# Optimization experiments

Hardware: AMD Instinct MI355X
Metric: run time of the kernel (lower is better)

Reference implementation:

```python
import jax, jax.numpy as jnp
import numpy as np

N_NODES = 50000
N_EDGES = 800000
IN_CH = 128
HID_CH = 8
OUT_CH = 64
HEADS = 32
NEG_SLOPE = 0.2  # PyG GATConv default


def setup_inputs() -> dict:
    key = jax.random.key(0)
    ks = jax.random.split(key, 12)
    x = jax.random.normal(ks[0], (N_NODES, IN_CH), dtype=jnp.float32)
    # edge_index with no self loops (src != dst), matching PyG's remove_self_loops
    src = jax.random.randint(ks[1], (N_EDGES,), 0, N_NODES)
    off = jax.random.randint(ks[2], (N_EDGES,), 1, N_NODES)
    dst = (src + off) % N_NODES
    edge_index = jnp.stack([src, dst]).astype(jnp.int64)
    s = 0.1
    W1 = jax.random.normal(ks[3], (IN_CH, HEADS * HID_CH), dtype=jnp.float32) * s
    att_src1 = jax.random.normal(ks[4], (HEADS, HID_CH), dtype=jnp.float32) * s
    att_dst1 = jax.random.normal(ks[5], (HEADS, HID_CH), dtype=jnp.float32) * s
    b1 = jnp.zeros((HEADS * HID_CH,), dtype=jnp.float32)
    W2 = jax.random.normal(ks[6], (HEADS * HID_CH, OUT_CH), dtype=jnp.float32) * s
    att_src2 = jax.random.normal(ks[7], (1, OUT_CH), dtype=jnp.float32) * s
    att_dst2 = jax.random.normal(ks[8], (1, OUT_CH), dtype=jnp.float32) * s
    b2 = jnp.zeros((OUT_CH,), dtype=jnp.float32)
    return {"x": x, "edge_index": edge_index, "W1": W1, "att_src1": att_src1,
            "att_dst1": att_dst1, "b1": b1, "W2": W2, "att_src2": att_src2,
            "att_dst2": att_dst2, "b2": b2}


def _gat_conv(x, src, dst, W, a_src, a_dst, bias, concat):
    # Faithful PyG GATConv: linear -> per-edge LeakyReLU score -> segment softmax over dst -> scatter-add
    n = x.shape[0]
    H, C = a_src.shape
    h = (x @ W).reshape(n, H, C)                      # [N,H,C]
    alpha_src = jnp.sum(h * a_src, axis=-1)           # [N,H]
    alpha_dst = jnp.sum(h * a_dst, axis=-1)           # [N,H]
    e = jax.nn.leaky_relu(alpha_src[src] + alpha_dst[dst], negative_slope=NEG_SLOPE)  # [E,H]
    e_max = jax.ops.segment_max(e, dst, num_segments=n)          # every node has a self loop
    ex = jnp.exp(e - e_max[dst])
    denom = jax.ops.segment_sum(ex, dst, num_segments=n)
    alpha = ex / (denom[dst] + 1e-16)                 # [E,H]
    msg = h[src] * alpha[:, :, None]                  # [E,H,C]
    out = jax.ops.segment_sum(msg, dst, num_segments=n)          # [N,H,C]
    out = out.reshape(n, H * C) if concat else out.mean(axis=1)
    return out + bias


def reference(x, edge_index, W1, att_src1, att_dst1, b1, W2, att_src2, att_dst2, b2):
    n = x.shape[0]
    loops = jnp.arange(n, dtype=edge_index.dtype)
    src = jnp.concatenate([edge_index[0], loops])     # add_self_loops (PyG default)
    dst = jnp.concatenate([edge_index[1], loops])
    h = _gat_conv(x, src, dst, W1, att_src1, att_dst1, b1, concat=True)
    h = _gat_conv(h, src, dst, W2, att_src2, att_dst2, b2, concat=False)
    return jax.nn.sigmoid(h)
```

## Files before the change

kernel.cpp:

```cpp
#include <hip/hip_runtime.h>
#include <hip/hip_bf16.h>

constexpr int N  = 50000;
constexpr int E  = 800000;
constexpr int F0 = 128;
constexpr int H1 = 32;
constexpr int F1 = 256;
constexpr int F2 = 64;
constexpr int NB = (N + 255) / 256;
constexpr int NPAD = 782 * 64;
constexpr int W1SZ = F0 * F1;
constexpr int W2SZ = F1 * F2;
constexpr float NEG_SLOPE = 0.2f;

typedef unsigned short u16;
typedef unsigned int   u32;
typedef __attribute__((ext_vector_type(8))) short bf16x8;
typedef __attribute__((ext_vector_type(4))) float f32x4;

__device__ __forceinline__ float leaky(float e) {
    return fmaxf(e, 0.f) + NEG_SLOPE * fminf(e, 0.f);
}
__device__ __forceinline__ float bf2f(u16 u) {
    u32 v = ((u32)u) << 16;
    return __builtin_bit_cast(float, v);
}
__device__ __forceinline__ u16 f2bf(float f) {
    u32 u = __builtin_bit_cast(u32, f);
    u += 0x7fffu + ((u >> 16) & 1u);
    return (u16)(u >> 16);
}
__device__ __forceinline__ u32 pack2(float a, float b) {
    return (u32)f2bf(a) | ((u32)f2bf(b) << 16);
}
__device__ __forceinline__ void up2(u32 v, float& lo, float& hi) {
    lo = __builtin_bit_cast(float, v << 16);
    hi = __builtin_bit_cast(float, v & 0xffff0000u);
}

__global__ void k_detect(const unsigned long long* __restrict__ p, int* __restrict__ flag) {
    __shared__ int bad;
    if (threadIdx.x == 0) bad = 0;
    __syncthreads();
    unsigned long long v = p[threadIdx.x];
    if (v >= (unsigned long long)N) atomicOr(&bad, 1);
    __syncthreads();
    if (threadIdx.x == 0) *flag = bad ? 0 : 1;
}
__device__ __forceinline__ int load_idx(const void* ei, long long i, int is64) {
    return is64 ? (int)((const long long*)ei)[i] : ((const int*)ei)[i];
}

__global__ void k_count(const void* __restrict__ ei, const int* __restrict__ flag,
                        int* __restrict__ deg) {
    int e = blockIdx.x * blockDim.x + threadIdx.x;
    if (e >= E) return;
    int dst = load_idx(ei, (long long)E + e, *flag);
    atomicAdd(&deg[dst], 1);
}
__global__ __launch_bounds__(256) void k_bsum(const int* __restrict__ deg, int* __restrict__ bsum) {
    int b = blockIdx.x, t = threadIdx.x, i = b * 256 + t;
    int v = (i < N) ? deg[i] : 0;
#pragma unroll
    for (int o = 1; o < 64; o <<= 1) v += __shfl_xor(v, o, 64);
    __shared__ int sw[4];
    if ((t & 63) == 0) sw[t >> 6] = v;
    __syncthreads();
    if (t == 0) bsum[b] = sw[0] + sw[1] + sw[2] + sw[3];
}
__global__ __launch_bounds__(256) void k_bscan(int* __restrict__ bsum, int* __restrict__ rsN) {
    int t = threadIdx.x, lane = t & 63, wy = t >> 6;
    int v = (t < NB) ? bsum[t] : 0;
    int inc = v;
#pragma unroll
    for (int o = 1; o < 64; o <<= 1) { int u = __shfl_up(inc, o, 64); if (lane >= o) inc += u; }
    __shared__ int wtot[4];
    if (lane == 63) wtot[wy] = inc;
    __syncthreads();
    int offs = 0;
    for (int k = 0; k < wy; k++) offs += wtot[k];
    int excl = offs + inc - v;
    if (t < NB) bsum[t] = excl;
    if (t == NB - 1) *rsN = excl + v;
}
__global__ __launch_bounds__(256) void k_rs(const int* __restrict__ deg,
                                            const int* __restrict__ bsum, int* __restrict__ rs) {
    int b = blockIdx.x, t = threadIdx.x, i = b * 256 + t;
    int lane = t & 63, wy = t >> 6;
    int v = (i < N) ? deg[i] : 0;
    int inc = v;
#pragma unroll
    for (int o = 1; o < 64; o <<= 1) { int u = __shfl_up(inc, o, 64); if (lane >= o) inc += u; }
    __shared__ int wtot[4];
    if (lane == 63) wtot[wy] = inc;
    __syncthreads();
    int offs = bsum[b];
    for (int k = 0; k < wy; k++) offs += wtot[k];
    if (i < N) rs[i] = offs + inc - v;
}
__global__ void k_scatter(const void* __restrict__ ei, const int* __restrict__ flag,
                          const int* __restrict__ rs, int* __restrict__ fill,
                          int* __restrict__ csr) {
    int e = blockIdx.x * blockDim.x + threadIdx.x;
    if (e >= E) return;
    int is64 = *flag;
    int src = load_idx(ei, e, is64);
    int dst = load_idx(ei, (long long)E + e, is64);
    int pos = rs[dst] + atomicAdd(&fill[dst], 1);
    csr[pos] = src;
}

__global__ __launch_bounds__(256) void k_prepw(
        const float* __restrict__ W1, const float* __restrict__ W2,
        u16* __restrict__ w1t, u16* __restrict__ w2t) {
    int i = blockIdx.x * 256 + threadIdx.x;
    if (i < W1SZ) {
        int n = i >> 7, k = i & 127;
        w1t[(n << 7) + (k ^ ((n & 7) << 3))] = f2bf(W1[k * F1 + n]);
    } else if (i < W1SZ + W2SZ) {
        int j = i - W1SZ;
        int n = j >> 8, k = j & 255;
        w2t[(n << 8) + (k ^ ((n & 7) << 3))] = f2bf(W2[k * F2 + n]);
    }
}

__global__ __launch_bounds__(256) void k_gemm1(
        const float* __restrict__ x, const u16* __restrict__ w1t, u16* __restrict__ h1b) {
    __shared__ u16 As[64 * 128];
    int r0 = blockIdx.x * 64;
    int t = threadIdx.x, w = t >> 6, l = t & 63;
    {
        int r = t >> 2, k0 = (t & 3) * 32, rr = r0 + r;
        int swz = (r & 7) << 3;
        float4 f[8];
        if (rr < N) {
            const float4* px = (const float4*)(x + (size_t)rr * F0 + k0);
#pragma unroll
            for (int j = 0; j < 8; j++) f[j] = px[j];
        } else {
#pragma unroll
            for (int j = 0; j < 8; j++) f[j] = make_float4(0.f, 0.f, 0.f, 0.f);
        }
#pragma unroll
        for (int g = 0; g < 4; g++) {
            uint4 st;
            st.x = pack2(f[2 * g].x, f[2 * g].y);
            st.y = pack2(f[2 * g].z, f[2 * g].w);
            st.z = pack2(f[2 * g + 1].x, f[2 * g + 1].y);
            st.w = pack2(f[2 * g + 1].z, f[2 * g + 1].w);
            *(uint4*)(As + r * 128 + ((k0 + 8 * g) ^ swz)) = st;
        }
    }
    bf16x8 bfrag[4][4];
#pragma unroll
    for (int n = 0; n < 4; n++) {
        int col = w * 64 + n * 16 + (l & 15);
        const u16* wrow = w1t + col * 128;
        int swz = (col & 7) << 3;
#pragma unroll
        for (int ks = 0; ks < 4; ks++)
            bfrag[n][ks] = *(const bf16x8*)(wrow + ((ks * 32 + (l >> 4) * 8) ^ swz));
    }
    __syncthreads();
    f32x4 z = {0.f, 0.f, 0.f, 0.f};
    f32x4 acc[4][4];
#pragma unroll
    for (int m = 0; m < 4; m++)
#pragma unroll
        for (int n = 0; n < 4; n++) acc[m][n] = z;
#pragma unroll
    for (int ks = 0; ks < 4; ks++) {
#pragma unroll
        for (int m = 0; m < 4; m++) {
            int row = m * 16 + (l & 15);
            bf16x8 a = *(const bf16x8*)(As + row * 128 +
                                        ((ks * 32 + (l >> 4) * 8) ^ ((row & 7) << 3)));
#pragma unroll
            for (int n = 0; n < 4; n++)
                acc[m][n] = __builtin_amdgcn_mfma_f32_16x16x32_bf16(a, bfrag[n][ks], acc[m][n], 0, 0, 0);
        }
    }
#pragma unroll
    for (int m = 0; m < 4; m++) {
        int rbase = r0 + m * 16 + (l >> 4) * 4;
#pragma unroll
        for (int n = 0; n < 4; n++) {
            int col = w * 64 + n * 16 + (l & 15);
#pragma unroll
            for (int r = 0; r < 4; r++) {
                int rr = rbase + r;
                if (rr < N) h1b[(size_t)rr * 256 + (col ^ ((rr & 7) << 3))] = f2bf(acc[m][n][r]);
            }
        }
    }
}

__global__ __launch_bounds__(256) void k_alpha1(
        const u16* __restrict__ h1b, const float* __restrict__ as1, const float* __restrict__ ad1,
        float* __restrict__ asrc1, float* __restrict__ adst1) {
    int row = blockIdx.x * 4 + (threadIdx.x >> 6);
    if (row >= N) return;
    int l = threadIdx.x & 63;
    int swz = (row & 7) << 3;
    uint2 v = *(const uint2*)(h1b + (size_t)row * 256 + 4 * l);
    int c0 = (4 * l) ^ swz;
    float f0, f1, f2, f3;
    up2(v.x, f0, f1); up2(v.y, f2, f3);
    float ps = f0 * as1[c0] + f1 * as1[c0 + 1] + f2 * as1[c0 + 2] + f3 * as1[c0 + 3];
    float pd = f0 * ad1[c0] + f1 * ad1[c0 + 1] + f2 * ad1[c0 + 2] + f3 * ad1[c0 + 3];
    ps += __shfl_xor(ps, 1, 64);
    pd += __shfl_xor(pd, 1, 64);
    if (!(l & 1)) {
        int head = (l >> 1) ^ (swz >> 3);
        asrc1[(size_t)row * H1 + head] = ps;
        adst1[(size_t)row * H1 + head] = pd;
    }
}

__global__ __launch_bounds__(256) void k_edge1(
        const int* __restrict__ rs, const int* __restrict__ csr,
        const u16* __restrict__ h1b, const float* __restrict__ asrc,
        const float* __restrict__ adst, const float* __restrict__ b1,
        u16* __restrict__ outb) {
    int d = blockIdx.x * 4 + (threadIdx.x >> 6);
    if (d >= N) return;
    int l = threadIdx.x & 63;
    int hl = l >> 1;
    int beg = rs[d], end = rs[d + 1];
    float ad_sc = adst[(size_t)d * H1 + (l & 31)];
    float wself = __expf(leaky(asrc[(size_t)d * H1 + hl] + adst[(size_t)d * H1 + hl]));
    float den = wself;
    int swzD = (d & 7) << 3;
    uint2 vd = *(const uint2*)(h1b + (size_t)d * 256 + ((4 * l) ^ swzD));
    float a0, a1, a2, a3;
    up2(vd.x, a0, a1); up2(vd.y, a2, a3);
    float c0 = wself * a0, c1 = wself * a1, c2 = wself * a2, c3 = wself * a3;

    for (int base = beg; base < end; base += 64) {
        int cnt = min(64, end - base);
        int s_ch = (base + l < end) ? csr[base + l] : 0;
        for (int i = 0; i < cnt; i += 2) {
            int sA = __shfl(s_ch, i, 64);
            int sB = __shfl(s_ch, i + 1, 64);
            int sS = (l < 32) ? sA : sB;
            float e = leaky(asrc[(size_t)sS * H1 + (l & 31)] + ad_sc);
            bool valid = (l < 32) | (i + 1 < cnt);
            float wsc = valid ? __expf(e) : 0.f;
            float wA = __shfl(wsc, hl, 64);
            float wB = __shfl(wsc, 32 + hl, 64);
            den += wA + wB;
            uint2 va = *(const uint2*)(h1b + (size_t)sA * 256 + ((4 * l) ^ ((sA & 7) << 3)));
            uint2 vb = *(const uint2*)(h1b + (size_t)sB * 256 + ((4 * l) ^ ((sB & 7) << 3)));
            float t0, t1, t2, t3;
            up2(va.x, t0, t1); up2(va.y, t2, t3);
            c0 = fmaf(wA, t0, c0); c1 = fmaf(wA, t1, c1);
            c2 = fmaf(wA, t2, c2); c3 = fmaf(wA, t3, c3);
            up2(vb.x, t0, t1); up2(vb.y, t2, t3);
            c0 = fmaf(wB, t0, c0); c1 = fmaf(wB, t1, c1);
            c2 = fmaf(wB, t2, c2); c3 = fmaf(wB, t3, c3);
        }
    }
    float inv = 1.f / (den + 1e-16f);
    int ch = 4 * l;
    uint2 st;
    st.x = pack2(c0 * inv + b1[ch], c1 * inv + b1[ch + 1]);
    st.y = pack2(c2 * inv + b1[ch + 2], c3 * inv + b1[ch + 3]);
    *(uint2*)(outb + (size_t)d * 256 + (ch ^ swzD)) = st;
}

__global__ __launch_bounds__(256) void k_gemm2(
        const u16* __restrict__ ab, const u16* __restrict__ w2t, u16* __restrict__ h2b) {
    __shared__ u16 As[64 * 256];
    int r0 = blockIdx.x * 64;
    int t = threadIdx.x, w = t >> 6, l = t & 63;
    {
        const uint4* gsrc = (const uint4*)(ab + (size_t)r0 * 256);
        uint4* lds = (uint4*)As;
        for (int i = t; i < 2048; i += 256) lds[i] = gsrc[i];
    }
    __syncthreads();
    f32x4 z = {0.f, 0.f, 0.f, 0.f};
    f32x4 acc[4];
#pragma unroll
    for (int n = 0; n < 4; n++) acc[n] = z;
    int row = w * 16 + (l & 15);
    int swzA = (row & 7) << 3;
#pragma unroll
    for (int ks = 0; ks < 8; ks++) {
        int ka = ks * 32 + (l >> 4) * 8;
        bf16x8 a = *(const bf16x8*)(As + row * 256 + (ka ^ swzA));
#pragma unroll
        for (int n = 0; n < 4; n++) {
            int col = n * 16 + (l & 15);
            bf16x8 b = *(const bf16x8*)(w2t + col * 256 + (ka ^ ((col & 7) << 3)));
            acc[n] = __builtin_amdgcn_mfma_f32_16x16x32_bf16(a, b, acc[n], 0, 0, 0);
        }
    }
#pragma unroll
    for (int n = 0; n < 4; n++) {
        int col = n * 16 + (l & 15);
#pragma unroll
        for (int r = 0; r < 4; r++) {
            int rr = r0 + w * 16 + (l >> 4) * 4 + r;
            if (rr < N) h2b[(size_t)rr * F2 + col] = f2bf(acc[n][r]);
        }
    }
}

__global__ __launch_bounds__(256) void k_alpha2(
        const u16* __restrict__ h2b, const float* __restrict__ a2s, const float* __restrict__ a2d,
        float* __restrict__ asrc2, float* __restrict__ adst2) {
    int row = blockIdx.x * 4 + (threadIdx.x >> 6);
    if (row >= N) return;
    int l = threadIdx.x & 63;
    float f = bf2f(h2b[(size_t)row * F2 + l]);
    float ps = f * a2s[l], pd = f * a2d[l];
#pragma unroll
    for (int o = 1; o < 64; o <<= 1) {
        ps += __shfl_xor(ps, o, 64);
        pd += __shfl_xor(pd, o, 64);
    }
    if (l == 0) { asrc2[row] = ps; adst2[row] = pd; }
}

__global__ __launch_bounds__(256) void k_edge2(
        const int* __restrict__ rs, const int* __restrict__ csr,
        const u16* __restrict__ h2b, const float* __restrict__ asrc,
        const float* __restrict__ adst, const float* __restrict__ b2,
        float* __restrict__ out) {
    int d = blockIdx.x * 4 + (threadIdx.x >> 6);
    if (d >= N) return;
    int l = threadIdx.x & 63;
    int q = l >> 4, c4 = (l & 15) * 4;
    int beg = rs[d], end = rs[d + 1];
    float add_ = adst[d];
    float wself = __expf(leaky(asrc[d] + add_));
    float wq0 = (q == 0) ? wself : 0.f;
    float den = wq0;
    uint2 vd = *(const uint2*)(h2b + (size_t)d * F2 + c4);
    float a0, a1, a2, a3;
    up2(vd.x, a0, a1); up2(vd.y, a2, a3);
    float c0 = wq0 * a0, c1 = wq0 * a1, c2 = wq0 * a2, c3 = wq0 * a3;

    for (int base = beg; base < end; base += 64) {
        int cnt = min(64, end - base);
        bool in = (base + l < end);
        int s_ch = in ? csr[base + l] : 0;
        float w_l = in ? __expf(leaky(asrc[s_ch] + add_)) : 0.f;
        for (int i = 0; i < cnt; i += 4) {
            int e = i + q;
            float wi = __shfl(w_l, e, 64);
            int   si = __shfl(s_ch, e, 64);
            wi = (e < cnt) ? wi : 0.f;
            uint2 v = *(const uint2*)(h2b + (size_t)si * F2 + c4);
            float t0, t1, t2, t3;
            up2(v.x, t0, t1); up2(v.y, t2, t3);
            c0 = fmaf(wi, t0, c0); c1 = fmaf(wi, t1, c1);
            c2 = fmaf(wi, t2, c2); c3 = fmaf(wi, t3, c3);
            den += wi;
        }
    }
    den += __shfl_xor(den, 16, 64); den += __shfl_xor(den, 32, 64);
    c0 += __shfl_xor(c0, 16, 64);   c0 += __shfl_xor(c0, 32, 64);
    c1 += __shfl_xor(c1, 16, 64);   c1 += __shfl_xor(c1, 32, 64);
    c2 += __shfl_xor(c2, 16, 64);   c2 += __shfl_xor(c2, 32, 64);
    c3 += __shfl_xor(c3, 16, 64);   c3 += __shfl_xor(c3, 32, 64);
    if (q == 0) {
        float inv = 1.f / (den + 1e-16f);
        float4 o;
        o.x = 1.f / (1.f + __expf(-(c0 * inv + b2[c4])));
        o.y = 1.f / (1.f + __expf(-(c1 * inv + b2[c4 + 1])));
        o.z = 1.f / (1.f + __expf(-(c2 * inv + b2[c4 + 2])));
        o.w = 1.f / (1.f + __expf(-(c3 * inv + b2[c4 + 3])));
        *(float4*)(out + (size_t)d * F2 + c4) = o;
    }
}

extern "C" void kernel_launch(void* const* d_in, const int* in_sizes, int n_in,
                              void* d_out, int out_size, void* d_ws, size_t ws_size,
                              hipStream_t stream) {
    const float* x   = (const float*)d_in[0];
    const void*  ei  = d_in[1];
    const float* W1  = (const float*)d_in[2];
    const float* as1 = (const float*)d_in[3];
    const float* ad1 = (const float*)d_in[4];
    const float* b1  = (const float*)d_in[5];
    const float* W2  = (const float*)d_in[6];
    const float* a2s = (const float*)d_in[7];
    const float* a2d = (const float*)d_in[8];
    const float* b2  = (const float*)d_in[9];
    float* out = (float*)d_out;

    char* wp = (char*)d_ws;
    size_t off = 0;
    auto alloc = [&](size_t bytes) {
        void* p = wp + off;
        off = (off + bytes + 255) & ~(size_t)255;
        return p;
    };
    int* flag  = (int*)alloc(4);
    int* deg   = (int*)alloc((size_t)N * 4);
    int* fill  = (int*)alloc((size_t)N * 4);
    int* rs    = (int*)alloc((size_t)(N + 1) * 4);
    int* bsum  = (int*)alloc((size_t)NB * 4);
    int* csr   = (int*)alloc((size_t)E * 4);
    u16* w1t   = (u16*)alloc((size_t)W1SZ * 2);
    u16* w2t   = (u16*)alloc((size_t)W2SZ * 2);
    u16* h1b   = (u16*)alloc((size_t)NPAD * F1 * 2);
    u16* h1ab  = (u16*)alloc((size_t)NPAD * F1 * 2);
    u16* h2b   = (u16*)alloc((size_t)NPAD * F2 * 2);
    float* asrc1 = (float*)alloc((size_t)N * H1 * 4);
    float* adst1 = (float*)alloc((size_t)N * H1 * 4);
    float* asrc2 = (float*)alloc((size_t)N * 4);
    float* adst2 = (float*)alloc((size_t)N * 4);

    hipMemsetAsync(deg, 0, (size_t)N * 4, stream);
    hipMemsetAsync(fill, 0, (size_t)N * 4, stream);

    k_detect<<<1, 1024, 0, stream>>>((const unsigned long long*)ei, flag);
    k_count<<<(E + 255) / 256, 256, 0, stream>>>(ei, flag, deg);
    k_bsum<<<NB, 256, 0, stream>>>(deg, bsum);
    k_bscan<<<1, 256, 0, stream>>>(bsum, rs + N);
    k_rs<<<NB, 256, 0, stream>>>(deg, bsum, rs);
    k_scatter<<<(E + 255) / 256, 256, 0, stream>>>(ei, flag, rs, fill, csr);

    k_prepw<<<(W1SZ + W2SZ + 255) / 256, 256, 0, stream>>>(W1, W2, w1t, w2t);
    k_gemm1<<<NPAD / 64, 256, 0, stream>>>(x, w1t, h1b);
    k_alpha1<<<(N + 3) / 4, 256, 0, stream>>>(h1b, as1, ad1, asrc1, adst1);
    k_edge1<<<(N + 3) / 4, 256, 0, stream>>>(rs, csr, h1b, asrc1, adst1, b1, h1ab);
    k_gemm2<<<NPAD / 64, 256, 0, stream>>>(h1ab, w2t, h2b);
    k_alpha2<<<(N + 3) / 4, 256, 0, stream>>>(h2b, a2s, a2d, asrc2, adst2);
    k_edge2<<<(N + 3) / 4, 256, 0, stream>>>(rs, csr, h2b, asrc2, adst2, b2, out);
}
```

Measured before the change: 246.2 us.

## Fuse attention-score dot products into GEMMs and simplify edge aggregation loops

Computes the per-node source/destination attention scores inside both GEMM epilogues from the fp32 accumulators, which removes the separate alpha1/alpha2 kernels and their re-reads of the bf16 features. The layer-1 edge loop now walks one neighbor at a time, using a wave-uniform readfirstlane index, instead of pairing two neighbors with shuffles. The layer-2 loop now reads csr directly with a stride of four rather than staging indices through shuffles. The CSR scatter uses a copied row-start array as an atomic cursor, which drops the fill memset and one load. The scores now come from unrounded accumulators, so values differ slightly from before. The GEMM epilogue also gains extra shuffle reductions.

New measurement: 296.0 us. 20.2% more time.

```diff
diff --git a/kernel.cpp b/kernel.cpp
--- a/kernel.cpp
+++ b/kernel.cpp
@@ -99,14 +99,13 @@
     if (i < N) rs[i] = offs + inc - v;
 }
 __global__ void k_scatter(const void* __restrict__ ei, const int* __restrict__ flag,
-                          const int* __restrict__ rs, int* __restrict__ fill,
-                          int* __restrict__ csr) {
+                          int* __restrict__ rs2, int* __restrict__ csr) {
     int e = blockIdx.x * blockDim.x + threadIdx.x;
     if (e >= E) return;
     int is64 = *flag;
     int src = load_idx(ei, e, is64);
     int dst = load_idx(ei, (long long)E + e, is64);
-    int pos = rs[dst] + atomicAdd(&fill[dst], 1);
+    int pos = atomicAdd(&rs2[dst], 1);
     csr[pos] = src;
 }
 
@@ -125,7 +124,9 @@
 }
 
 __global__ __launch_bounds__(256) void k_gemm1(
-        const float* __restrict__ x, const u16* __restrict__ w1t, u16* __restrict__ h1b) {
+        const float* __restrict__ x, const u16* __restrict__ w1t,
+        const float* __restrict__ as1, const float* __restrict__ ad1,
+        u16* __restrict__ h1b, float* __restrict__ asrc1, float* __restrict__ adst1) {
     __shared__ u16 As[64 * 128];
     int r0 = blockIdx.x * 64;
     int t = threadIdx.x, w = t >> 6, l = t & 63;
@@ -193,27 +194,34 @@
             }
         }
     }
-}
-
-__global__ __launch_bounds__(256) void k_alpha1(
-        const u16* __restrict__ h1b, const float* __restrict__ as1, const float* __restrict__ ad1,
-        float* __restrict__ asrc1, float* __restrict__ adst1) {
-    int row = blockIdx.x * 4 + (threadIdx.x >> 6);
-    if (row >= N) return;
-    int l = threadIdx.x & 63;
-    int swz = (row & 7) << 3;
-    uint2 v = *(const uint2*)(h1b + (size_t)row * 256 + 4 * l);
-    int c0 = (4 * l) ^ swz;
-    float f0, f1, f2, f3;
-    up2(v.x, f0, f1); up2(v.y, f2, f3);
-    float ps = f0 * as1[c0] + f1 * as1[c0 + 1] + f2 * as1[c0 + 2] + f3 * as1[c0 + 3];
-    float pd = f0 * ad1[c0] + f1 * ad1[c0 + 1] + f2 * ad1[c0 + 2] + f3 * ad1[c0 + 3];
-    ps += __shfl_xor(ps, 1, 64);
-    pd += __shfl_xor(pd, 1, 64);
-    if (!(l & 1)) {
-        int head = (l >> 1) ^ (swz >> 3);
-        asrc1[(size_t)row * H1 + head] = ps;
-        adst1[(size_t)row * H1 + head] = pd;
+    float as1v[4], ad1v[4];
+#pragma unroll
+    for (int n = 0; n < 4; n++) {
+        int col = w * 64 + n * 16 + (l & 15);
+        as1v[n] = as1[col];
+        ad1v[n] = ad1[col];
+    }
+#pragma unroll
+    for (int m = 0; m < 4; m++) {
+#pragma unroll
+        for (int r = 0; r < 4; r++) {
+            int row = r0 + m * 16 + (l >> 4) * 4 + r;
+#pragma unroll
+            for (int n = 0; n < 4; n++) {
+                float ps = acc[m][n][r] * as1v[n];
+                float pd = acc[m][n][r] * ad1v[n];
+#pragma unroll
+                for (int o = 1; o < 8; o <<= 1) {
+                    ps += __shfl_xor(ps, o, 64);
+                    pd += __shfl_xor(pd, o, 64);
+                }
+                if ((l & 7) == 0 && row < N) {
+                    int head = w * 8 + n * 2 + ((l >> 3) & 1);
+                    asrc1[(size_t)row * H1 + head] = ps;
+                    adst1[(size_t)row * H1 + head] = pd;
+                }
+            }
+        }
     }
 }
 
@@ -227,49 +235,38 @@
     int l = threadIdx.x & 63;
     int hl = l >> 1;
     int beg = rs[d], end = rs[d + 1];
-    float ad_sc = adst[(size_t)d * H1 + (l & 31)];
-    float wself = __expf(leaky(asrc[(size_t)d * H1 + hl] + adst[(size_t)d * H1 + hl]));
+    float ad_hl = adst[(size_t)d * H1 + hl];
+    float wself = __expf(leaky(asrc[(size_t)d * H1 + hl] + ad_hl));
     float den = wself;
     int swzD = (d & 7) << 3;
-    uint2 vd = *(const uint2*)(h1b + (size_t)d * 256 + ((4 * l) ^ swzD));
+    int ch4 = 4 * l;
+    uint2 vd = *(const uint2*)(h1b + (size_t)d * 256 + (ch4 ^ swzD));
     float a0, a1, a2, a3;
     up2(vd.x, a0, a1); up2(vd.y, a2, a3);
     float c0 = wself * a0, c1 = wself * a1, c2 = wself * a2, c3 = wself * a3;
 
-    for (int base = beg; base < end; base += 64) {
-        int cnt = min(64, end - base);
-        int s_ch = (base + l < end) ? csr[base + l] : 0;
-        for (int i = 0; i < cnt; i += 2) {
-            int sA = __shfl(s_ch, i, 64);
-            int sB = __shfl(s_ch, i + 1, 64);
-            int sS = (l < 32) ? sA : sB;
-            float e = leaky(asrc[(size_t)sS * H1 + (l & 31)] + ad_sc);
-            bool valid = (l < 32) | (i + 1 < cnt);
-            float wsc = valid ? __expf(e) : 0.f;
-            float wA = __shfl(wsc, hl, 64);
-            float wB = __shfl(wsc, 32 + hl, 64);
-            den += wA + wB;
-            uint2 va = *(const uint2*)(h1b + (size_t)sA * 256 + ((4 * l) ^ ((sA & 7) << 3)));
-            uint2 vb = *(const uint2*)(h1b + (size_t)sB * 256 + ((4 * l) ^ ((sB & 7) << 3)));
-            float t0, t1, t2, t3;
-            up2(va.x, t0, t1); up2(va.y, t2, t3);
-            c0 = fmaf(wA, t0, c0); c1 = fmaf(wA, t1, c1);
-            c2 = fmaf(wA, t2, c2); c3 = fmaf(wA, t3, c3);
-            up2(vb.x, t0, t1); up2(vb.y, t2, t3);
-            c0 = fmaf(wB, t0, c0); c1 = fmaf(wB, t1, c1);
-            c2 = fmaf(wB, t2, c2); c3 = fmaf(wB, t3, c3);
-        }
+#pragma unroll 4
+    for (int i = beg; i < end; ++i) {
+        int s = __builtin_amdgcn_readfirstlane(csr[i]);
+        float wv = __expf(leaky(asrc[(size_t)s * H1 + hl] + ad_hl));
+        uint2 v = *(const uint2*)(h1b + (size_t)s * 256 + (ch4 ^ ((s & 7) << 3)));
+        den += wv;
+        float t0, t1, t2, t3;
+        up2(v.x, t0, t1); up2(v.y, t2, t3);
+        c0 = fmaf(wv, t0, c0); c1 = fmaf(wv, t1, c1);
+        c2 = fmaf(wv, t2, c2); c3 = fmaf(wv, t3, c3);
     }
     float inv = 1.f / (den + 1e-16f);
-    int ch = 4 * l;
     uint2 st;
-    st.x = pack2(c0 * inv + b1[ch], c1 * inv + b1[ch + 1]);
-    st.y = pack2(c2 * inv + b1[ch + 2], c3 * inv + b1[ch + 3]);
-    *(uint2*)(outb + (size_t)d * 256 + (ch ^ swzD)) = st;
+    st.x = pack2(c0 * inv + b1[ch4], c1 * inv + b1[ch4 + 1]);
+    st.y = pack2(c2 * inv + b1[ch4 + 2], c3 * inv + b1[ch4 + 3]);
+    *(uint2*)(outb + (size_t)d * 256 + (ch4 ^ swzD)) = st;
 }
 
 __global__ __launch_bounds__(256) void k_gemm2(
-        const u16* __restrict__ ab, const u16* __restrict__ w2t, u16* __restrict__ h2b) {
+        const u16* __restrict__ ab, const u16* __restrict__ w2t,
+        const float* __restrict__ a2s, const float* __restrict__ a2d,
+        u16* __restrict__ h2b, float* __restrict__ asrc2, float* __restrict__ adst2) {
     __shared__ u16 As[64 * 256];
     int r0 = blockIdx.x * 64;
     int t = threadIdx.x, w = t >> 6, l = t & 63;
@@ -305,22 +302,28 @@
             if (rr < N) h2b[(size_t)rr * F2 + col] = f2bf(acc[n][r]);
         }
     }
-}
-
-__global__ __launch_bounds__(256) void k_alpha2(
-        const u16* __restrict__ h2b, const float* __restrict__ a2s, const float* __restrict__ a2d,
-        float* __restrict__ asrc2, float* __restrict__ adst2) {
-    int row = blockIdx.x * 4 + (threadIdx.x >> 6);
-    if (row >= N) return;
-    int l = threadIdx.x & 63;
-    float f = bf2f(h2b[(size_t)row * F2 + l]);
-    float ps = f * a2s[l], pd = f * a2d[l];
-#pragma unroll
-    for (int o = 1; o < 64; o <<= 1) {
-        ps += __shfl_xor(ps, o, 64);
-        pd += __shfl_xor(pd, o, 64);
-    }
-    if (l == 0) { asrc2[row] = ps; adst2[row] = pd; }
+    float a2sv[4], a2dv[4];
+#pragma unroll
+    for (int n = 0; n < 4; n++) {
+        a2sv[n] = a2s[n * 16 + (l & 15)];
+        a2dv[n] = a2d[n * 16 + (l & 15)];
+    }
+#pragma unroll
+    for (int r = 0; r < 4; r++) {
+        int rr = r0 + w * 16 + (l >> 4) * 4 + r;
+        float ps = 0.f, pd = 0.f;
+#pragma unroll
+        for (int n = 0; n < 4; n++) {
+            ps = fmaf(acc[n][r], a2sv[n], ps);
+            pd = fmaf(acc[n][r], a2dv[n], pd);
+        }
+#pragma unroll
+        for (int o = 1; o < 16; o <<= 1) {
+            ps += __shfl_xor(ps, o, 64);
+            pd += __shfl_xor(pd, o, 64);
+        }
+        if ((l & 15) == 0 && rr < N) { asrc2[rr] = ps; adst2[rr] = pd; }
+    }
 }
 
 __global__ __launch_bounds__(256) void k_edge2(
@@ -342,23 +345,15 @@
     up2(vd.x, a0, a1); up2(vd.y, a2, a3);
     float c0 = wq0 * a0, c1 = wq0 * a1, c2 = wq0 * a2, c3 = wq0 * a3;
 
-    for (int base = beg; base < end; base += 64) {
-        int cnt = min(64, end - base);
-        bool in = (base + l < end);
-        int s_ch = in ? csr[base + l] : 0;
-        float w_l = in ? __expf(leaky(asrc[s_ch] + add_)) : 0.f;
-        for (int i = 0; i < cnt; i += 4) {
-            int e = i + q;
-            float wi = __shfl(w_l, e, 64);
-            int   si = __shfl(s_ch, e, 64);
-            wi = (e < cnt) ? wi : 0.f;
-            uint2 v = *(const uint2*)(h2b + (size_t)si * F2 + c4);
-            float t0, t1, t2, t3;
-            up2(v.x, t0, t1); up2(v.y, t2, t3);
-            c0 = fmaf(wi, t0, c0); c1 = fmaf(wi, t1, c1);
-            c2 = fmaf(wi, t2, c2); c3 = fmaf(wi, t3, c3);
-            den += wi;
-        }
+    for (int i = beg + q; i < end; i += 4) {
+        int s = csr[i];
+        float wv = __expf(leaky(asrc[s] + add_));
+        uint2 v = *(const uint2*)(h2b + (size_t)s * F2 + c4);
+        den += wv;
+        float t0, t1, t2, t3;
+        up2(v.x, t0, t1); up2(v.y, t2, t3);
+        c0 = fmaf(wv, t0, c0); c1 = fmaf(wv, t1, c1);
+        c2 = fmaf(wv, t2, c2); c3 = fmaf(wv, t3, c3);
     }
     den += __shfl_xor(den, 16, 64); den += __shfl_xor(den, 32, 64);
     c0 += __shfl_xor(c0, 16, 64);   c0 += __shfl_xor(c0, 32, 64);
@@ -400,8 +395,8 @@
     };
     int* flag  = (int*)alloc(4);
     int* deg   = (int*)alloc((size_t)N * 4);
-    int* fill  = (int*)alloc((size_t)N * 4);
     int* rs    = (int*)alloc((size_t)(N + 1) * 4);
+    int* rs2   = (int*)alloc((size_t)N * 4);
     int* bsum  = (int*)alloc((size_t)NB * 4);
     int* csr   = (int*)alloc((size_t)E * 4);
     u16* w1t   = (u16*)alloc((size_t)W1SZ * 2);
@@ -415,20 +410,18 @@
     float* adst2 = (float*)alloc((size_t)N * 4);
 
     hipMemsetAsync(deg, 0, (size_t)N * 4, stream);
-    hipMemsetAsync(fill, 0, (size_t)N * 4, stream);
 
     k_detect<<<1, 1024, 0, stream>>>((const unsigned long long*)ei, flag);
     k_count<<<(E + 255) / 256, 256, 0, stream>>>(ei, flag, deg);
     k_bsum<<<NB, 256, 0, stream>>>(deg, bsum);
     k_bscan<<<1, 256, 0, stream>>>(bsum, rs + N);
     k_rs<<<NB, 256, 0, stream>>>(deg, bsum, rs);
-    k_scatter<<<(E + 255) / 256, 256, 0, stream>>>(ei, flag, rs, fill, csr);
+    hipMemcpyAsync(rs2, rs, (size_t)N * 4, hipMemcpyDeviceToDevice, stream);
+    k_scatter<<<(E + 255) / 256, 256, 0, stream>>>(ei, flag, rs2, csr);
 
     k_prepw<<<(W1SZ + W2SZ + 255) / 256, 256, 0, stream>>>(W1, W2, w1t, w2t);
-    k_gemm1<<<NPAD / 64, 256, 0, stream>>>(x, w1t, h1b);
-    k_alpha1<<<(N + 3) / 4, 256, 0, stream>>>(h1b, as1, ad1, asrc1, adst1);
+    k_gemm1<<<NPAD / 64, 256, 0, stream>>>(x, w1t, as1, ad1, h1b, asrc1, adst1);
     k_edge1<<<(N + 3) / 4, 256, 0, stream>>>(rs, csr, h1b, asrc1, adst1, b1, h1ab);
-    k_gemm2<<<NPAD / 64, 256, 0, stream>>>(h1ab, w2t, h2b);
-    k_alpha2<<<(N + 3) / 4, 256, 0, stream>>>(h2b, a2s, a2d, asrc2, adst2);
+    k_gemm2<<<NPAD / 64, 256, 0, stream>>>(h1ab, w2t, a2s, a2d, h2b, asrc2, adst2);
     k_edge2<<<(N + 3) / 4, 256, 0, stream>>>(rs, csr, h2b, asrc2, adst2, b2, out);
 }
```
